# Optimization experiments

Hardware: AMD Instinct MI355X
Metric: run time of the kernel (lower is better)

The kernel has to match this reference:

```python
import jax, jax.numpy as jnp
import numpy as np

EPS = 1e-12  # F.normalize eps

def _l2norm(x, axis=-1):
    n = jnp.sqrt(jnp.sum(x * x, axis=axis, keepdims=True))
    return x / jnp.maximum(n, EPS)

def setup_inputs() -> dict:
    key = jax.random.key(0)
    k1, k2 = jax.random.split(key)
    N, D, C = 262144, 128, 1024
    embeddings = jax.random.normal(k1, (N, D), dtype=jnp.float32)
    labels = jax.random.randint(k2, (N,), 0, C, dtype=jnp.int64)
    return {"embeddings": embeddings, "labels": labels, "num_classes": C}

def reference(embeddings, labels, num_classes):
    # Normalize all embeddings: [N, D]
    emb = _l2norm(embeddings, axis=1)
    # Per-class segment sums and counts (replaces python loop over unique labels)
    sums = jax.ops.segment_sum(emb, labels, num_segments=num_classes)          # [C, D]
    counts = jax.ops.segment_sum(jnp.ones((emb.shape[0],), emb.dtype), labels,
                                 num_segments=num_classes)                     # [C]
    safe_counts = jnp.maximum(counts, 1.0)
    prototypes = _l2norm(sums / safe_counts[:, None], axis=1)                  # [C, D]
    # cosine sim of each sample to its class prototype
    sim = jnp.sum(emb * prototypes[labels], axis=1)                           # [N]
    # per-class mean of (1 - sim)
    loss_sums = jax.ops.segment_sum(1.0 - sim, labels, num_segments=num_classes)
    per_class = loss_sums / safe_counts                                        # [C]
    valid = (counts >= 2.0).astype(emb.dtype)                                  # classes with >=2 samples
    n_valid = jnp.sum(valid)
    loss = jnp.sum(per_class * valid) / jnp.maximum(n_valid, 1.0)
    return jnp.where(n_valid > 0, loss, jnp.zeros((), emb.dtype))
```

## Files before the change

### kernel.cpp

```cpp
#include <hip/hip_runtime.h>
#include <math.h>

#define NUM_CLASSES 1024
#define HIST_CHUNK 2048
#define NB 128

__device__ __forceinline__ int detect_mode32(const int* __restrict__ l) {
    return (l[1] | l[3] | l[5] | l[7] | l[9] | l[11] | l[13] | l[15]) != 0;
}
__device__ __forceinline__ int get_label(const int* __restrict__ l, int i, int mode32) {
    return l[mode32 ? i : (i << 1)] & (NUM_CLASSES - 1);
}
__device__ __forceinline__ unsigned bf16rne(float x) {
    unsigned u = __float_as_uint(x);
    return (u + 0x7FFFu + ((u >> 16) & 1u)) >> 16;
}
__device__ __forceinline__ unsigned packbf(float a, float b) {
    return bf16rne(a) | (bf16rne(b) << 16);
}
__device__ __forceinline__ float unpack_lo(unsigned u) { return __uint_as_float(u << 16); }
__device__ __forceinline__ float unpack_hi(unsigned u) { return __uint_as_float(u & 0xffff0000u); }

__global__ void hist_kernel(const int* __restrict__ labels, int n,
                            int* __restrict__ pT) {
    __shared__ int h[NUM_CLASSES];
    const int mode32 = detect_mode32(labels);
    for (int i = threadIdx.x; i < NUM_CLASSES; i += blockDim.x) h[i] = 0;
    __syncthreads();
    const int base = blockIdx.x * HIST_CHUNK;
    for (int k = threadIdx.x; k < HIST_CHUNK; k += blockDim.x) {
        int i = base + k;
        if (i < n) atomicAdd(&h[get_label(labels, i, mode32)], 1);
    }
    __syncthreads();
    for (int c = threadIdx.x; c < NUM_CLASSES; c += blockDim.x)
        pT[c * NB + blockIdx.x] = h[c];
}

__global__ __launch_bounds__(512) void scanA_kernel(int* __restrict__ pT,
                                                    int* __restrict__ totals) {
    const int wave = threadIdx.x >> 6;
    const int lane = threadIdx.x & 63;
    const int c = blockIdx.x * 8 + wave;
    int* p = pT + c * NB;
    const int v0 = p[2 * lane];
    const int v1 = p[2 * lane + 1];
    int s = v0 + v1;
    #pragma unroll
    for (int d = 1; d < 64; d <<= 1) {
        int t = __shfl_up(s, d, 64);
        if (lane >= d) s += t;
    }
    const int base = s - v0 - v1;
    p[2 * lane]     = base;
    p[2 * lane + 1] = base + v0;
    if (lane == 63) totals[c] = s;
}

__global__ void scanB_kernel(const int* __restrict__ totals,
                             int* __restrict__ offsets,
                             int* __restrict__ counts,
                             float* __restrict__ accum,
                             int* __restrict__ ticket) {
    __shared__ int tmp[NUM_CLASSES];
    const int c = threadIdx.x;
    const int v = totals[c];
    tmp[c] = v;
    __syncthreads();
    for (int off = 1; off < NUM_CLASSES; off <<= 1) {
        int add = (c >= off) ? tmp[c - off] : 0;
        __syncthreads();
        tmp[c] += add;
        __syncthreads();
    }
    offsets[c] = tmp[c] - v;
    counts[c]  = v;
    if (c == 0) { accum[0] = 0.0f; accum[1] = 0.0f; *ticket = 0; }
}

__global__ void rank_kernel(const int* __restrict__ labels, int n,
                            const int* __restrict__ pT,
                            const int* __restrict__ offsets,
                            int* __restrict__ rank) {
    __shared__ int cur[NUM_CLASSES];
    const int mode32 = detect_mode32(labels);
    for (int c = threadIdx.x; c < NUM_CLASSES; c += blockDim.x)
        cur[c] = offsets[c] + pT[c * NB + blockIdx.x];
    __syncthreads();
    const int base = blockIdx.x * HIST_CHUNK;
    for (int k = threadIdx.x; k < HIST_CHUNK; k += blockDim.x) {
        int i = base + k;
        if (i < n)
            rank[i] = atomicAdd(&cur[get_label(labels, i, mode32)], 1);
    }
}

__global__ __launch_bounds__(512) void norm_scatter_kernel(
        const float* __restrict__ emb,
        const int* __restrict__ rank,
        uint4* __restrict__ nbuf,
        int n) {
    const int wave = threadIdx.x >> 6;
    const int lane = threadIdx.x & 63;
    const int g    = lane >> 4;
    const int sub  = lane & 15;
    const int base = blockIdx.x * 256;

    for (int r = wave * 4 + g; r < 256; r += 32) {
        const int row = base + r;
        if (row < n) {
            const float4* rp = (const float4*)(emb + (size_t)row * 128);
            float4 v0 = rp[sub];
            float4 v1 = rp[sub + 16];
            float sq = v0.x*v0.x + v0.y*v0.y + v0.z*v0.z + v0.w*v0.w
                     + v1.x*v1.x + v1.y*v1.y + v1.z*v1.z + v1.w*v1.w;
            sq += __shfl_xor(sq, 1, 64);
            sq += __shfl_xor(sq, 2, 64);
            sq += __shfl_xor(sq, 4, 64);
            sq += __shfl_xor(sq, 8, 64);
            float inv = 1.0f / fmaxf(sqrtf(sq), 1e-12f);
            uint4 w;
            w.x = packbf(v0.x * inv, v0.y * inv);
            w.y = packbf(v0.z * inv, v0.w * inv);
            w.z = packbf(v1.x * inv, v1.y * inv);
            w.w = packbf(v1.z * inv, v1.w * inv);
            const int pos = rank[row];
            nbuf[(size_t)pos * 16 + sub] = w;
        }
    }
}

#define WPB 8
__global__ __launch_bounds__(512) void class_sum2_kernel(
        const uint4* __restrict__ nbuf,
        const int* __restrict__ offsets,
        const int* __restrict__ counts,
        float* __restrict__ accum,
        int* __restrict__ ticket,
        float* __restrict__ out) {
    const int c     = blockIdx.x;
    const int start = offsets[c];
    const int count = counts[c];
    const int wave  = threadIdx.x >> 6;
    const int lane  = threadIdx.x & 63;
    const int g     = lane >> 4;
    const int sub   = lane & 15;

    float a[8];
    #pragma unroll
    for (int j = 0; j < 8; j++) a[j] = 0.0f;

    for (int r = wave * 4 + g; r < count; r += WPB * 4) {
        const uint4 w = nbuf[(size_t)(start + r) * 16 + sub];
        a[0] += unpack_lo(w.x); a[1] += unpack_hi(w.x);
        a[2] += unpack_lo(w.y); a[3] += unpack_hi(w.y);
        a[4] += unpack_lo(w.z); a[5] += unpack_hi(w.z);
        a[6] += unpack_lo(w.w); a[7] += unpack_hi(w.w);
    }

    __shared__ float s[WPB * 4][16][8];
    {
        float* dst = s[wave * 4 + g][sub];
        #pragma unroll
        for (int j = 0; j < 8; j++) dst[j] = a[j];
    }
    __syncthreads();

    __shared__ float red[128];
    if (threadIdx.x < 128) {
        const int d  = threadIdx.x;
        const int sb = d >> 3;
        const int j  = d & 7;
        float t = 0.0f;
        #pragma unroll
        for (int k = 0; k < WPB * 4; k++) t += s[k][sb][j];
        red[d] = t * t;
    }
    __syncthreads();
    if (threadIdx.x < 64) {
        float x = red[threadIdx.x] + red[threadIdx.x + 64];
        #pragma unroll
        for (int off = 32; off; off >>= 1) x += __shfl_xor(x, off, 64);
        if (threadIdx.x == 0) {
            if (count >= 2) {
                float nrm = sqrtf(x);
                float per_class = ((float)count - nrm) / (float)count;
                atomicAdd(&accum[0], per_class);
                atomicAdd(&accum[1], 1.0f);
            }
            __threadfence();
            int old = atomicAdd(ticket, 1);
            if (old == NUM_CLASSES - 1) {
                float ls = atomicAdd(&accum[0], 0.0f);
                float nv = atomicAdd(&accum[1], 0.0f);
                out[0] = (nv > 0.0f) ? (ls / nv) : 0.0f;
            }
        }
    }
}

extern "C" void kernel_launch(void* const* d_in, const int* in_sizes, int n_in,
                              void* d_out, int out_size, void* d_ws, size_t ws_size,
                              hipStream_t stream) {
    const float* emb  = (const float*)d_in[0];
    const int* labels = (const int*)d_in[1];
    const int n = in_sizes[1];

    char* ws = (char*)d_ws;
    int*   counts  = (int*)(ws + 0);
    int*   offsets = (int*)(ws + 4096);
    int*   totals  = (int*)(ws + 8192);
    float* accum   = (float*)(ws + 12288);
    int*   ticket  = (int*)(ws + 12304);
    int*   rank    = (int*)(ws + 16384);
    int*   pT      = (int*)(ws + 16384 + (size_t)n * 4);
    uint4* nbuf    = (uint4*)(ws + (2u << 20));

    const int normBlocks = (n + 255) / 256;

    hist_kernel <<<NB, 256, 0, stream>>>(labels, n, pT);
    scanA_kernel<<<NB, 512, 0, stream>>>(pT, totals);
    scanB_kernel<<<1, NUM_CLASSES, 0, stream>>>(totals, offsets, counts, accum, ticket);
    rank_kernel <<<NB, 256, 0, stream>>>(labels, n, pT, offsets, rank);
    norm_scatter_kernel<<<normBlocks, 512, 0, stream>>>(emb, rank, nbuf, n);
    class_sum2_kernel<<<NUM_CLASSES, 512, 0, stream>>>(nbuf, offsets, counts,
                                                       accum, ticket, (float*)d_out);
}
```

Before: 273.4 us.

## Replace per-class counting sort with 8-bucket scatter and LDS atomic bucket sums

The full per-class counting sort (rank kernel plus two-level scan) becomes a coarse 8-bucket sort. The norm/scatter kernel now takes slot positions from shared-memory atomics and stores a per-row byte class slot. A new bucket-sum kernel accumulates rows into a 128x128 LDS tile with float atomics, and a combine kernel reduces 64 partial tiles per bucket. This removes the rank pass and the imbalance of one block per class, at the cost of LDS atomic contention, a 32 MB partials buffer, and nondeterministic summation order.

```diff
diff --git a/kernel.cpp b/kernel.cpp
--- a/kernel.cpp
+++ b/kernel.cpp
@@ -2,8 +2,9 @@
 #include <math.h>
 
 #define NUM_CLASSES 1024
-#define HIST_CHUNK 2048
-#define NB 128
+#define NB 256
+#define NSB 512
+#define BPB 64
 
 __device__ __forceinline__ int detect_mode32(const int* __restrict__ l) {
     return (l[1] | l[3] | l[5] | l[7] | l[9] | l[11] | l[13] | l[15]) != 0;
@@ -21,94 +22,94 @@
 __device__ __forceinline__ float unpack_lo(unsigned u) { return __uint_as_float(u << 16); }
 __device__ __forceinline__ float unpack_hi(unsigned u) { return __uint_as_float(u & 0xffff0000u); }
 
-__global__ void hist_kernel(const int* __restrict__ labels, int n,
-                            int* __restrict__ pT) {
+__global__ void hist_kernel(const int* __restrict__ labels, int n, int chunk,
+                            int* __restrict__ pT,
+                            int* __restrict__ bh) {
     __shared__ int h[NUM_CLASSES];
     const int mode32 = detect_mode32(labels);
     for (int i = threadIdx.x; i < NUM_CLASSES; i += blockDim.x) h[i] = 0;
     __syncthreads();
-    const int base = blockIdx.x * HIST_CHUNK;
-    for (int k = threadIdx.x; k < HIST_CHUNK; k += blockDim.x) {
+    const int base = blockIdx.x * chunk;
+    for (int k = threadIdx.x; k < chunk; k += blockDim.x) {
         int i = base + k;
         if (i < n) atomicAdd(&h[get_label(labels, i, mode32)], 1);
     }
     __syncthreads();
     for (int c = threadIdx.x; c < NUM_CLASSES; c += blockDim.x)
         pT[c * NB + blockIdx.x] = h[c];
-}
-
-__global__ __launch_bounds__(512) void scanA_kernel(int* __restrict__ pT,
-                                                    int* __restrict__ totals) {
+    if (threadIdx.x < 8) {
+        int s = 0;
+        #pragma unroll 16
+        for (int k = 0; k < 128; k++) s += h[threadIdx.x * 128 + k];
+        bh[threadIdx.x * NB + blockIdx.x] = s;
+    }
+}
+
+__global__ void counts_kernel(const int* __restrict__ pT, int* __restrict__ counts) {
+    const int c = blockIdx.x * 128 + threadIdx.x;
+    int s = 0;
+    for (int b = 0; b < NB; b++) s += pT[c * NB + b];
+    counts[c] = s;
+}
+
+__global__ __launch_bounds__(1024) void scanBH_kernel(int* __restrict__ bh,
+        int* __restrict__ meta,
+        float* __restrict__ accum, int* __restrict__ ticket) {
+    __shared__ int tmp[1024];
+    __shared__ int base[9];
+    const int t = threadIdx.x;
+    const int q = t >> 7, j = t & 127;
+    const int a0 = bh[q * NB + 2 * j];
+    const int a1 = bh[q * NB + 2 * j + 1];
+    const int s = a0 + a1;
+    tmp[t] = s;
+    __syncthreads();
+    for (int off = 1; off < 128; off <<= 1) {
+        int add = (j >= off) ? tmp[t - off] : 0;
+        __syncthreads();
+        tmp[t] += add;
+        __syncthreads();
+    }
+    if (t == 0) {
+        base[0] = 0;
+        for (int qq = 0; qq < 8; qq++) {
+            int tot = tmp[qq * 128 + 127];
+            meta[8 + qq] = tot;
+            meta[qq] = base[qq];
+            base[qq + 1] = base[qq] + tot;
+        }
+        accum[0] = 0.0f; accum[1] = 0.0f; *ticket = 0;
+    }
+    __syncthreads();
+    const int pairExcl = tmp[t] - s;
+    bh[q * NB + 2 * j]     = base[q] + pairExcl;
+    bh[q * NB + 2 * j + 1] = base[q] + pairExcl + a0;
+}
+
+__global__ __launch_bounds__(512) void norm_scatter_kernel(
+        const float* __restrict__ emb, const int* __restrict__ labels,
+        int n, int chunk,
+        const int* __restrict__ bh,
+        uint4* __restrict__ nbuf,
+        unsigned char* __restrict__ slot8) {
+    __shared__ int cur[8];
+    const int mode32 = detect_mode32(labels);
+    if (threadIdx.x < 8) cur[threadIdx.x] = bh[threadIdx.x * NB + blockIdx.x];
+    __syncthreads();
+    const int lane = threadIdx.x & 63;
     const int wave = threadIdx.x >> 6;
-    const int lane = threadIdx.x & 63;
-    const int c = blockIdx.x * 8 + wave;
-    int* p = pT + c * NB;
-    const int v0 = p[2 * lane];
-    const int v1 = p[2 * lane + 1];
-    int s = v0 + v1;
-    #pragma unroll
-    for (int d = 1; d < 64; d <<= 1) {
-        int t = __shfl_up(s, d, 64);
-        if (lane >= d) s += t;
-    }
-    const int base = s - v0 - v1;
-    p[2 * lane]     = base;
-    p[2 * lane + 1] = base + v0;
-    if (lane == 63) totals[c] = s;
-}
-
-__global__ void scanB_kernel(const int* __restrict__ totals,
-                             int* __restrict__ offsets,
-                             int* __restrict__ counts,
-                             float* __restrict__ accum,
-                             int* __restrict__ ticket) {
-    __shared__ int tmp[NUM_CLASSES];
-    const int c = threadIdx.x;
-    const int v = totals[c];
-    tmp[c] = v;
-    __syncthreads();
-    for (int off = 1; off < NUM_CLASSES; off <<= 1) {
-        int add = (c >= off) ? tmp[c - off] : 0;
-        __syncthreads();
-        tmp[c] += add;
-        __syncthreads();
-    }
-    offsets[c] = tmp[c] - v;
-    counts[c]  = v;
-    if (c == 0) { accum[0] = 0.0f; accum[1] = 0.0f; *ticket = 0; }
-}
-
-__global__ void rank_kernel(const int* __restrict__ labels, int n,
-                            const int* __restrict__ pT,
-                            const int* __restrict__ offsets,
-                            int* __restrict__ rank) {
-    __shared__ int cur[NUM_CLASSES];
-    const int mode32 = detect_mode32(labels);
-    for (int c = threadIdx.x; c < NUM_CLASSES; c += blockDim.x)
-        cur[c] = offsets[c] + pT[c * NB + blockIdx.x];
-    __syncthreads();
-    const int base = blockIdx.x * HIST_CHUNK;
-    for (int k = threadIdx.x; k < HIST_CHUNK; k += blockDim.x) {
-        int i = base + k;
-        if (i < n)
-            rank[i] = atomicAdd(&cur[get_label(labels, i, mode32)], 1);
-    }
-}
-
-__global__ __launch_bounds__(512) void norm_scatter_kernel(
-        const float* __restrict__ emb,
-        const int* __restrict__ rank,
-        uint4* __restrict__ nbuf,
-        int n) {
-    const int wave = threadIdx.x >> 6;
-    const int lane = threadIdx.x & 63;
     const int g    = lane >> 4;
     const int sub  = lane & 15;
-    const int base = blockIdx.x * 256;
-
-    for (int r = wave * 4 + g; r < 256; r += 32) {
+    const int base = blockIdx.x * chunk;
+
+    for (int r = wave * 4 + g; r < chunk; r += 32) {
         const int row = base + r;
         if (row < n) {
+            const int lab = get_label(labels, row, mode32);
+            const int q = lab >> 7;
+            int pos = 0;
+            if (sub == 0) pos = atomicAdd(&cur[q], 1);
+            pos = __shfl(pos, lane & ~15, 64);
             const float4* rp = (const float4*)(emb + (size_t)row * 128);
             float4 v0 = rp[sub];
             float4 v1 = rp[sub + 16];
@@ -124,77 +125,75 @@
             w.y = packbf(v0.z * inv, v0.w * inv);
             w.z = packbf(v1.x * inv, v1.y * inv);
             w.w = packbf(v1.z * inv, v1.w * inv);
-            const int pos = rank[row];
             nbuf[(size_t)pos * 16 + sub] = w;
-        }
-    }
-}
-
-#define WPB 8
-__global__ __launch_bounds__(512) void class_sum2_kernel(
-        const uint4* __restrict__ nbuf,
-        const int* __restrict__ offsets,
+            if (sub == 0) slot8[pos] = (unsigned char)(lab & 127);
+        }
+    }
+}
+
+__global__ __launch_bounds__(512) void bucket_sum_kernel(
+        const unsigned* __restrict__ nbuf32,
+        const unsigned char* __restrict__ slot8,
+        const int* __restrict__ meta,
+        float* __restrict__ partials) {
+    __shared__ float L[128 * 128];
+    for (int t = threadIdx.x; t < 128 * 128; t += blockDim.x) L[t] = 0.0f;
+    __syncthreads();
+    const int q = blockIdx.x >> 6;
+    const int j = blockIdx.x & (BPB - 1);
+    const int tot = meta[8 + q];
+    const int chunk = (tot + BPB - 1) / BPB;
+    const int lo = meta[q] + j * chunk;
+    const int hi = min(lo + chunk, meta[q] + tot);
+    const int wave = threadIdx.x >> 6;
+    const int lane = threadIdx.x & 63;
+
+    for (int row = lo + wave; row < hi; row += 8) {
+        const int slot = slot8[row];
+        const unsigned u = nbuf32[(size_t)row * 64 + lane];
+        atomicAdd(&L[slot * 128 + 2 * lane],     unpack_lo(u));
+        atomicAdd(&L[slot * 128 + 2 * lane + 1], unpack_hi(u));
+    }
+    __syncthreads();
+    float* dst = partials + (size_t)blockIdx.x * 128 * 128;
+    for (int t = threadIdx.x; t < 128 * 128; t += blockDim.x) dst[t] = L[t];
+}
+
+__global__ __launch_bounds__(128) void combine_kernel(
+        const float* __restrict__ partials,
         const int* __restrict__ counts,
-        float* __restrict__ accum,
-        int* __restrict__ ticket,
+        float* __restrict__ accum, int* __restrict__ ticket,
         float* __restrict__ out) {
-    const int c     = blockIdx.x;
-    const int start = offsets[c];
-    const int count = counts[c];
-    const int wave  = threadIdx.x >> 6;
-    const int lane  = threadIdx.x & 63;
-    const int g     = lane >> 4;
-    const int sub   = lane & 15;
-
-    float a[8];
+    const int c = blockIdx.x;
+    const int q = c >> 7;
+    const int slot = c & 127;
+    const int t = threadIdx.x;
+    float s = 0.0f;
+    #pragma unroll 8
+    for (int b = 0; b < BPB; b++)
+        s += partials[((size_t)(q * BPB + b) * 128 + slot) * 128 + t];
+    float x = s * s;
     #pragma unroll
-    for (int j = 0; j < 8; j++) a[j] = 0.0f;
-
-    for (int r = wave * 4 + g; r < count; r += WPB * 4) {
-        const uint4 w = nbuf[(size_t)(start + r) * 16 + sub];
-        a[0] += unpack_lo(w.x); a[1] += unpack_hi(w.x);
-        a[2] += unpack_lo(w.y); a[3] += unpack_hi(w.y);
-        a[4] += unpack_lo(w.z); a[5] += unpack_hi(w.z);
-        a[6] += unpack_lo(w.w); a[7] += unpack_hi(w.w);
-    }
-
-    __shared__ float s[WPB * 4][16][8];
-    {
-        float* dst = s[wave * 4 + g][sub];
-        #pragma unroll
-        for (int j = 0; j < 8; j++) dst[j] = a[j];
-    }
-    __syncthreads();
-
-    __shared__ float red[128];
-    if (threadIdx.x < 128) {
-        const int d  = threadIdx.x;
-        const int sb = d >> 3;
-        const int j  = d & 7;
-        float t = 0.0f;
-        #pragma unroll
-        for (int k = 0; k < WPB * 4; k++) t += s[k][sb][j];
-        red[d] = t * t;
-    }
-    __syncthreads();
-    if (threadIdx.x < 64) {
-        float x = red[threadIdx.x] + red[threadIdx.x + 64];
-        #pragma unroll
-        for (int off = 32; off; off >>= 1) x += __shfl_xor(x, off, 64);
-        if (threadIdx.x == 0) {
-            if (count >= 2) {
-                float nrm = sqrtf(x);
-                float per_class = ((float)count - nrm) / (float)count;
-                atomicAdd(&accum[0], per_class);
-                atomicAdd(&accum[1], 1.0f);
-            }
-            __threadfence();
-            int old = atomicAdd(ticket, 1);
-            if (old == NUM_CLASSES - 1) {
-                float ls = atomicAdd(&accum[0], 0.0f);
-                float nv = atomicAdd(&accum[1], 0.0f);
-                out[0] = (nv > 0.0f) ? (ls / nv) : 0.0f;
-            }
+    for (int off = 32; off; off >>= 1) x += __shfl_xor(x, off, 64);
+    __shared__ float r2[2];
+    const int lane = t & 63;
+    if (lane == 0) r2[t >> 6] = x;
+    __syncthreads();
+    if (t == 0) {
+        float tot = r2[0] + r2[1];
+        const int count = counts[c];
+        if (count >= 2) {
+            float nrm = sqrtf(tot);
+            float per_class = ((float)count - nrm) / (float)count;
+            atomicAdd(&accum[0], per_class);
+            atomicAdd(&accum[1], 1.0f);
+        }
+        __threadfence();
+        int old = atomicAdd(ticket, 1);
+        if (old == NUM_CLASSES - 1) {
+            float ls = atomicAdd(&accum[0], 0.0f);
+            float nv = atomicAdd(&accum[1], 0.0f);
+            out[0] = (nv > 0.0f) ? (ls / nv) : 0.0f;
         }
     }
 }
@@ -205,24 +204,24 @@
     const float* emb  = (const float*)d_in[0];
     const int* labels = (const int*)d_in[1];
     const int n = in_sizes[1];
+    const int chunk = (n + NB - 1) / NB;
 
     char* ws = (char*)d_ws;
     int*   counts  = (int*)(ws + 0);
-    int*   offsets = (int*)(ws + 4096);
-    int*   totals  = (int*)(ws + 8192);
-    float* accum   = (float*)(ws + 12288);
-    int*   ticket  = (int*)(ws + 12304);
-    int*   rank    = (int*)(ws + 16384);
-    int*   pT      = (int*)(ws + 16384 + (size_t)n * 4);
-    uint4* nbuf    = (uint4*)(ws + (2u << 20));
-
-    const int normBlocks = (n + 255) / 256;
-
-    hist_kernel <<<NB, 256, 0, stream>>>(labels, n, pT);
-    scanA_kernel<<<NB, 512, 0, stream>>>(pT, totals);
-    scanB_kernel<<<1, NUM_CLASSES, 0, stream>>>(totals, offsets, counts, accum, ticket);
-    rank_kernel <<<NB, 256, 0, stream>>>(labels, n, pT, offsets, rank);
-    norm_scatter_kernel<<<normBlocks, 512, 0, stream>>>(emb, rank, nbuf, n);
-    class_sum2_kernel<<<NUM_CLASSES, 512, 0, stream>>>(nbuf, offsets, counts,
-                                                       accum, ticket, (float*)d_out);
-}
+    int*   bh      = (int*)(ws + 4096);
+    int*   meta    = (int*)(ws + 12352);
+    float* accum   = (float*)(ws + 12480);
+    int*   ticket  = (int*)(ws + 12496);
+    int*   pT      = (int*)(ws + 16384);
+    unsigned char* slot8 = (unsigned char*)(ws + (2u << 20));
+    uint4* nbuf    = (uint4*)(ws + (4u << 20));
+    float* partials= (float*)(ws + (72u << 20));
+
+    hist_kernel  <<<NB, 256, 0, stream>>>(labels, n, chunk, pT, bh);
+    counts_kernel<<<8, 128, 0, stream>>>(pT, counts);
+    scanBH_kernel<<<1, 1024, 0, stream>>>(bh, meta, accum, ticket);
+    norm_scatter_kernel<<<NB, 512, 0, stream>>>(emb, labels, n, chunk, bh, nbuf, slot8);
+    bucket_sum_kernel<<<NSB, 512, 0, stream>>>((const unsigned*)nbuf, slot8, meta, partials);
+    combine_kernel<<<NUM_CLASSES, 128, 0, stream>>>(partials, counts, accum, ticket,
+                                                    (float*)d_out);
+}
```

Result: slower. 446.4 us (+63.3%).

## Write normalized rows sequentially and gather by sorted index in class sum

Applied to the files above, without the earlier changes.

The normalize kernel now writes bf16 rows in their original order instead of scattering them to class-sorted positions. The rank array becomes a sorted index list, which the class-sum kernel uses to gather rows: each wave reads one full 256-byte row, two rows per iteration. This trades scattered 16-byte writes for coalesced writes plus an indirect gather on the read side. It also simplifies the per-wave accumulators and the shared-memory reduction.

```diff
diff --git a/kernel.cpp b/kernel.cpp
--- a/kernel.cpp
+++ b/kernel.cpp
@@ -78,10 +78,10 @@
     if (c == 0) { accum[0] = 0.0f; accum[1] = 0.0f; *ticket = 0; }
 }
 
-__global__ void rank_kernel(const int* __restrict__ labels, int n,
-                            const int* __restrict__ pT,
-                            const int* __restrict__ offsets,
-                            int* __restrict__ rank) {
+__global__ void scatter_kernel(const int* __restrict__ labels, int n,
+                               const int* __restrict__ pT,
+                               const int* __restrict__ offsets,
+                               int* __restrict__ sorted) {
     __shared__ int cur[NUM_CLASSES];
     const int mode32 = detect_mode32(labels);
     for (int c = threadIdx.x; c < NUM_CLASSES; c += blockDim.x)
@@ -90,14 +90,15 @@
     const int base = blockIdx.x * HIST_CHUNK;
     for (int k = threadIdx.x; k < HIST_CHUNK; k += blockDim.x) {
         int i = base + k;
-        if (i < n)
-            rank[i] = atomicAdd(&cur[get_label(labels, i, mode32)], 1);
-    }
-}
-
-__global__ __launch_bounds__(512) void norm_scatter_kernel(
+        if (i < n) {
+            int pos = atomicAdd(&cur[get_label(labels, i, mode32)], 1);
+            sorted[pos] = i;
+        }
+    }
+}
+
+__global__ __launch_bounds__(512) void norm_seq_kernel(
         const float* __restrict__ emb,
-        const int* __restrict__ rank,
         uint4* __restrict__ nbuf,
         int n) {
     const int wave = threadIdx.x >> 6;
@@ -124,15 +125,15 @@
             w.y = packbf(v0.z * inv, v0.w * inv);
             w.z = packbf(v1.x * inv, v1.y * inv);
             w.w = packbf(v1.z * inv, v1.w * inv);
-            const int pos = rank[row];
-            nbuf[(size_t)pos * 16 + sub] = w;
+            nbuf[(size_t)row * 16 + sub] = w;
         }
     }
 }
 
 #define WPB 8
-__global__ __launch_bounds__(512) void class_sum2_kernel(
-        const uint4* __restrict__ nbuf,
+__global__ __launch_bounds__(512) void class_sum_kernel(
+        const unsigned* __restrict__ nbuf32,
+        const int* __restrict__ sorted,
         const int* __restrict__ offsets,
         const int* __restrict__ counts,
         float* __restrict__ accum,
@@ -143,38 +144,38 @@
     const int count = counts[c];
     const int wave  = threadIdx.x >> 6;
     const int lane  = threadIdx.x & 63;
-    const int g     = lane >> 4;
-    const int sub   = lane & 15;
-
-    float a[8];
-    #pragma unroll
-    for (int j = 0; j < 8; j++) a[j] = 0.0f;
-
-    for (int r = wave * 4 + g; r < count; r += WPB * 4) {
-        const uint4 w = nbuf[(size_t)(start + r) * 16 + sub];
-        a[0] += unpack_lo(w.x); a[1] += unpack_hi(w.x);
-        a[2] += unpack_lo(w.y); a[3] += unpack_hi(w.y);
-        a[4] += unpack_lo(w.z); a[5] += unpack_hi(w.z);
-        a[6] += unpack_lo(w.w); a[7] += unpack_hi(w.w);
-    }
-
-    __shared__ float s[WPB * 4][16][8];
-    {
-        float* dst = s[wave * 4 + g][sub];
-        #pragma unroll
-        for (int j = 0; j < 8; j++) dst[j] = a[j];
-    }
+
+    float a0 = 0.0f, a1 = 0.0f;
+    int r = wave;
+    for (; r + WPB < count; r += 2 * WPB) {
+        const int i0 = sorted[start + r];
+        const int i1 = sorted[start + r + WPB];
+        const unsigned u0 = nbuf32[(size_t)i0 * 64 + lane];
+        const unsigned u1 = nbuf32[(size_t)i1 * 64 + lane];
+        a0 += unpack_lo(u0); a1 += unpack_hi(u0);
+        a0 += unpack_lo(u1); a1 += unpack_hi(u1);
+    }
+    if (r < count) {
+        const int i0 = sorted[start + r];
+        const unsigned u0 = nbuf32[(size_t)i0 * 64 + lane];
+        a0 += unpack_lo(u0); a1 += unpack_hi(u0);
+    }
+
+    __shared__ float2 s2[WPB][64];
+    s2[wave][lane] = make_float2(a0, a1);
     __syncthreads();
 
     __shared__ float red[128];
     if (threadIdx.x < 128) {
-        const int d  = threadIdx.x;
-        const int sb = d >> 3;
-        const int j  = d & 7;
+        int l = threadIdx.x >> 1;
+        int hi = threadIdx.x & 1;
         float t = 0.0f;
         #pragma unroll
-        for (int k = 0; k < WPB * 4; k++) t += s[k][sb][j];
-        red[d] = t * t;
+        for (int w = 0; w < WPB; w++) {
+            float2 v = s2[w][l];
+            t += hi ? v.y : v.x;
+        }
+        red[threadIdx.x] = t * t;
     }
     __syncthreads();
     if (threadIdx.x < 64) {
@@ -212,17 +213,16 @@
     int*   totals  = (int*)(ws + 8192);
     float* accum   = (float*)(ws + 12288);
     int*   ticket  = (int*)(ws + 12304);
-    int*   rank    = (int*)(ws + 16384);
+    int*   sorted  = (int*)(ws + 16384);
     int*   pT      = (int*)(ws + 16384 + (size_t)n * 4);
-    uint4* nbuf    = (uint4*)(ws + (2u << 20));
-
-    const int normBlocks = (n + 255) / 256;
+    uint4* nbuf    = (uint4*)(ws + (4u << 20));
 
     hist_kernel <<<NB, 256, 0, stream>>>(labels, n, pT);
     scanA_kernel<<<NB, 512, 0, stream>>>(pT, totals);
     scanB_kernel<<<1, NUM_CLASSES, 0, stream>>>(totals, offsets, counts, accum, ticket);
-    rank_kernel <<<NB, 256, 0, stream>>>(labels, n, pT, offsets, rank);
-    norm_scatter_kernel<<<normBlocks, 512, 0, stream>>>(emb, rank, nbuf, n);
-    class_sum2_kernel<<<NUM_CLASSES, 512, 0, stream>>>(nbuf, offsets, counts,
-                                                       accum, ticket, (float*)d_out);
-}
+    scatter_kernel<<<NB, 256, 0, stream>>>(labels, n, pT, offsets, sorted);
+    norm_seq_kernel<<<(n + 255) / 256, 512, 0, stream>>>(emb, nbuf, n);
+    class_sum_kernel<<<NUM_CLASSES, 512, 0, stream>>>((const unsigned*)nbuf, sorted,
+                                                      offsets, counts,
+                                                      accum, ticket, (float*)d_out);
+}
```

After: 275.7 us. No clear change (+0.8%).
